# Performance work log

Measured on AMD Instinct MI355X. Metric: run time of the kernel, lower is better.

Reference implementation:

```python
import jax, jax.numpy as jnp
import numpy as np

B = 4096
D0, D1 = 256, 64


def setup_inputs() -> dict:
    key = jax.random.key(0)
    k0, k1, k2, k3 = jax.random.split(key, 4)
    return {
        "s0": jax.random.normal(k0, (B, D0), dtype=jnp.float32),
        "s1": jax.random.normal(k1, (B, D1), dtype=jnp.float32),
        "t0": jax.random.normal(k2, (B, D0), dtype=jnp.float32),
        "t1": jax.random.normal(k3, (B, D1), dtype=jnp.float32),
    }


def _gaussian_kernel(source, target):
    # feats: [2B, D]
    feats = jnp.concatenate([source, target], axis=0)
    n = feats.shape[0]
    # pairwise squared distances [2B, 2B] via the Gram-matrix identity
    # (same math as ((x - y) ** 2).sum(-1), avoids the [N, N, D] intermediate)
    sq = jnp.sum(feats * feats, axis=-1)
    dist = sq[:, None] + sq[None, :] - 2.0 * (feats @ feats.T)
    # median-heuristic bandwidth with num_kernels=1: gamma = (n^2 - n) / sum(dist)
    gamma = (n * n - n) / jnp.sum(jax.lax.stop_gradient(dist))
    return jnp.exp(-dist * gamma)


def reference(s0, s1, t0, t1):
    # joint kernel: elementwise product of per-stream Gaussian kernels
    k = _gaussian_kernel(s0, t0) * _gaussian_kernel(s1, t1)
    b = s0.shape[0]
    s2s = k[:b, :b]
    t2t = k[b:, b:]
    s2t = k[:b, b:]
    return jnp.mean(s2s + t2t - 2.0 * s2t)
```

## Files before the change

### kernel.cpp

```cpp
#include <hip/hip_runtime.h>
#include <hip/hip_fp8.h>

#define B_ROWS 4096
#define NTOT   8192
#define D0     256
#define D1     64
#define KDIM   320
#define NSB    128
#define NTILE  64
#define NTRI   2080

typedef __attribute__((ext_vector_type(4))) float f32x4;
typedef __attribute__((ext_vector_type(2))) long long2v;

#define OFF_GAM   0
#define OFF_PQ0   32
#define OFF_PQ1   544
#define OFF_P0    1056
#define OFF_P1    132128
#define OFF_R0    164896
#define OFF_R1    197664
#define OFF_BSUM  230432
#define OFF_PHI   247072

__device__ __forceinline__ void load_lds16(const void* g, void* l) {
    __builtin_amdgcn_global_load_lds(
        (const __attribute__((address_space(1))) void*)g,
        (__attribute__((address_space(3))) void*)l, 16, 0, 0);
}

__global__ __launch_bounds__(256) void k_prep(
    const float* __restrict__ s0, const float* __restrict__ s1,
    const float* __restrict__ t0, const float* __restrict__ t1,
    float* __restrict__ part0, float* __restrict__ part1,
    float* __restrict__ pq0, float* __restrict__ pq1,
    unsigned char* __restrict__ phi,
    float* __restrict__ r0vec, float* __restrict__ r1vec) {
    __shared__ float sh0[4][256];
    __shared__ float sh1[4][64];
    __shared__ float shq[4][2];
    int t = threadIdx.x, wv = t >> 6, lane = t & 63;
    int rb = blockIdx.x * 64;
    int c4 = lane * 4;
    int rr = wv;

    f32x4 cs = {0.f, 0.f, 0.f, 0.f};
    float q0 = 0.f;
    #pragma unroll 4
    for (int k = 0; k < 16; ++k) {
        int row = rb + rr + k * 4;
        const float* b0 = (row < B_ROWS) ? s0 + (size_t)row * D0 : t0 + (size_t)(row - B_ROWS) * D0;
        f32x4 v = *(const f32x4*)(b0 + c4);
        cs.x += v.x; cs.y += v.y; cs.z += v.z; cs.w += v.w;
        q0 += v.x * v.x + v.y * v.y + v.z * v.z + v.w * v.w;
    }
    *(f32x4*)&sh0[rr][c4] = cs;

    float cs1 = 0.f, q1 = 0.f;
    #pragma unroll 4
    for (int k = 0; k < 16; ++k) {
        int row = rb + rr + k * 4;
        const float* b1 = (row < B_ROWS) ? s1 + (size_t)row * D1 : t1 + (size_t)(row - B_ROWS) * D1;
        float v = b1[lane];
        cs1 += v; q1 += v * v;
    }
    sh1[rr][lane] = cs1;

    #pragma unroll
    for (int o = 32; o; o >>= 1) { q0 += __shfl_xor(q0, o, 64); q1 += __shfl_xor(q1, o, 64); }
    if (lane == 0) { shq[wv][0] = q0; shq[wv][1] = q1; }
    __syncthreads();

    part0[blockIdx.x * D0 + t] = sh0[0][t] + sh0[1][t] + sh0[2][t] + sh0[3][t];
    if (t < D1) part1[blockIdx.x * D1 + t] = sh1[0][t] + sh1[1][t] + sh1[2][t] + sh1[3][t];
    if (t == 0) {
        pq0[blockIdx.x] = shq[0][0] + shq[1][0] + shq[2][0] + shq[3][0];
        pq1[blockIdx.x] = shq[0][1] + shq[1][1] + shq[2][1] + shq[3][1];
    }

    for (int r = 0; r < 16; ++r) {
        int row = rb + wv * 16 + r;
        const float* b0p = (row < B_ROWS) ? s0 + (size_t)row * D0
                                          : t0 + (size_t)(row - B_ROWS) * D0;
        const float* b1p = (row < B_ROWS) ? s1 + (size_t)row * D1
                                          : t1 + (size_t)(row - B_ROWS) * D1;
        unsigned char* pr = phi + (size_t)row * KDIM;
        f32x4 v = *(const f32x4*)(b0p + lane * 4);
        __hip_fp8_e4m3 a0(v.x), a1(v.y), a2(v.z), a3(v.w);
        unsigned int word = (unsigned int)a0.__x | ((unsigned int)a1.__x << 8) |
                            ((unsigned int)a2.__x << 16) | ((unsigned int)a3.__x << 24);
        int doff0 = ((lane >> 4) << 6) + (((lane >> 1) & 3) << 4) +
                    (((lane >> 3) & 1) << 3) + ((lane & 1) << 2);
        *(unsigned int*)(pr + doff0) = word;
        float f0 = (float)a0, f1 = (float)a1, f2 = (float)a2, f3 = (float)a3;
        float p0 = f0 * f0 + f1 * f1 + f2 * f2 + f3 * f3;
        __hip_fp8_e4m3 qd(b1p[lane]);
        int doff1 = 256 + (((lane >> 3) & 3) << 4) + (((lane >> 5) & 1) << 3) + (lane & 7);
        pr[doff1] = qd.__x;
        float fd = (float)qd;
        float p1 = fd * fd;
        #pragma unroll
        for (int o = 32; o; o >>= 1) { p0 += __shfl_xor(p0, o, 64); p1 += __shfl_xor(p1, o, 64); }
        if (lane == 0) { r0vec[row] = p0; r1vec[row] = p1; }
    }
}

__global__ __launch_bounds__(256) void k_gamma(
    const float* __restrict__ pq0, const float* __restrict__ pq1,
    const float* __restrict__ part0, const float* __restrict__ part1,
    float* __restrict__ gam) {
    __shared__ double sh[4][4];
    int t = threadIdx.x, wv = t >> 6, lane = t & 63;

    double a0 = 0.0, a1 = 0.0;
    if (t < NSB) { a0 = (double)pq0[t]; a1 = (double)pq1[t]; }

    double F0t = 0.0;
    for (int b = 0; b < NSB; ++b) F0t += (double)part0[b * D0 + t];
    double nf0 = F0t * F0t;

    double nf1 = 0.0;
    if (t < D1) {
        double F1t = 0.0;
        for (int b = 0; b < NSB; ++b) F1t += (double)part1[b * D1 + t];
        nf1 = F1t * F1t;
    }

    #pragma unroll
    for (int o = 32; o; o >>= 1) {
        a0  += __shfl_xor(a0, o, 64);
        a1  += __shfl_xor(a1, o, 64);
        nf0 += __shfl_xor(nf0, o, 64);
        nf1 += __shfl_xor(nf1, o, 64);
    }
    if (lane == 0) { sh[wv][0] = a0; sh[wv][1] = a1; sh[wv][2] = nf0; sh[wv][3] = nf1; }
    __syncthreads();
    if (t == 0) {
        double b0 = 0, b1 = 0, b2 = 0, b3 = 0;
        for (int w = 0; w < 4; ++w) { b0 += sh[w][0]; b1 += sh[w][1]; b2 += sh[w][2]; b3 += sh[w][3]; }
        double n = (double)NTOT;
        double g0 = (n * n - n) / (2.0 * n * b0 - 2.0 * b2);
        double g1 = (n * n - n) / (2.0 * n * b1 - 2.0 * b3);
        gam[0] = (float)g0; gam[1] = (float)g1;
        gam[2] = (float)(g1 / g0); gam[3] = (float)(2.0 * g0);
    }
}

__global__ __launch_bounds__(256, 3) void k_mmd(
    const unsigned char* __restrict__ phi,
    const float* __restrict__ r0vec, const float* __restrict__ r1vec,
    const float* __restrict__ gam, double* __restrict__ blocksum) {
    int tb = (blockIdx.x & 7) * (NTRI / 8) + (blockIdx.x >> 3);
    int I = (int)((129.0f - sqrtf(16641.0f - 8.0f * (float)tb)) * 0.5f);
    while ((129 * I - I * I) / 2 > tb) --I;
    while ((129 * (I + 1) - (I + 1) * (I + 1)) / 2 <= tb) ++I;
    int J = I + (tb - (129 * I - I * I) / 2);

    __shared__ unsigned char As[24576];
    __shared__ unsigned char Bs[24576];
    __shared__ float wsum[4];

    int tid = threadIdx.x, wv = tid >> 6, lane = tid & 63;
    int wr = wv >> 1, wc = wv & 1;
    int rgrp = lane >> 4, rlow = lane & 15;
    const int rowA = I * 128, rowB = J * 128;

    const float g0 = gam[0], g1 = gam[1], ratio = gam[2], tg0 = gam[3];

    f32x4 acc_[4][4] = {};

    #define STAGE(tbase, nt)                                                    \
        _Pragma("unroll")                                                       \
        for (int it = 0; it < (nt) * 2; ++it) {                                 \
            int idx = it * 256 + tid;                                           \
            int tt = idx >> 9, rs = idx & 511;                                  \
            int row = rs >> 2, slot = rs & 3;                                   \
            int rg = slot ^ ((row >> 1) & 3);                                   \
            size_t gcol = ((tbase) + tt) * 64 + rg * 16;                        \
            load_lds16(phi + (size_t)(rowA + row) * KDIM + gcol,                \
                       As + it * 4096 + wv * 1024);                             \
            load_lds16(phi + (size_t)(rowB + row) * KDIM + gcol,                \
                       Bs + it * 4096 + wv * 1024);                             \
        }

    #define LOADFRAG(tt)                                                        \
        long2v af[4], bf[4];                                                    \
        _Pragma("unroll")                                                       \
        for (int m = 0; m < 4; ++m) {                                           \
            int row = wr * 64 + m * 16 + rlow;                                  \
            int sl = rgrp ^ ((row >> 1) & 3);                                   \
            af[m] = *(const long2v*)&As[(tt) * 8192 + row * 64 + sl * 16];      \
        }                                                                       \
        _Pragma("unroll")                                                       \
        for (int n = 0; n < 4; ++n) {                                           \
            int col = wc * 64 + n * 16 + rlow;                                  \
            int sl = rgrp ^ ((col >> 1) & 3);                                   \
            bf[n] = *(const long2v*)&Bs[(tt) * 8192 + col * 64 + sl * 16];      \
        }

    STAGE(0, 3);
    __syncthreads();
    #pragma unroll
    for (int tt = 0; tt < 3; ++tt) {
        LOADFRAG(tt);
        __builtin_amdgcn_s_setprio(1);
        #pragma unroll
        for (int m = 0; m < 4; ++m)
            #pragma unroll
            for (int n = 0; n < 4; ++n) {
                acc_[m][n] = __builtin_amdgcn_mfma_f32_16x16x32_fp8_fp8(
                    af[m][0], bf[n][0], acc_[m][n], 0, 0, 0);
                acc_[m][n] = __builtin_amdgcn_mfma_f32_16x16x32_fp8_fp8(
                    af[m][1], bf[n][1], acc_[m][n], 0, 0, 0);
            }
        __builtin_amdgcn_s_setprio(0);
    }
    __syncthreads();
    STAGE(3, 2);
    __syncthreads();
    {
        LOADFRAG(0);
        __builtin_amdgcn_s_setprio(1);
        #pragma unroll
        for (int m = 0; m < 4; ++m)
            #pragma unroll
            for (int n = 0; n < 4; ++n) {
                acc_[m][n] = __builtin_amdgcn_mfma_f32_16x16x32_fp8_fp8(
                    af[m][0], bf[n][0], acc_[m][n], 0, 0, 0);
                acc_[m][n] = __builtin_amdgcn_mfma_f32_16x16x32_fp8_fp8(
                    af[m][1], bf[n][1], acc_[m][n], 0, 0, 0);
            }
        __builtin_amdgcn_s_setprio(0);
    }
    {
        LOADFRAG(1);
        __builtin_amdgcn_s_setprio(1);
        #pragma unroll
        for (int m = 0; m < 4; ++m)
            #pragma unroll
            for (int n = 0; n < 4; ++n) {
                f32x4 tm = {0.f, 0.f, 0.f, 0.f};
                tm = __builtin_amdgcn_mfma_f32_16x16x32_fp8_fp8(
                    af[m][0], bf[n][0], tm, 0, 0, 0);
                tm = __builtin_amdgcn_mfma_f32_16x16x32_fp8_fp8(
                    af[m][1], bf[n][1], tm, 0, 0, 0);
                acc_[m][n] += ratio * tm;
            }
        __builtin_amdgcn_s_setprio(0);
    }

    float psum = 0.f;
    #pragma unroll
    for (int m = 0; m < 4; ++m) {
        int gi = rowA + wr * 64 + m * 16 + rgrp * 4;
        f32x4 r0i = *(const f32x4*)&r0vec[gi];
        f32x4 r1i = *(const f32x4*)&r1vec[gi];
        f32x4 ui = g0 * r0i + g1 * r1i;
        #pragma unroll
        for (int n = 0; n < 4; ++n) {
            int gj = rowB + wc * 64 + n * 16 + rlow;
            float uj = g0 * r0vec[gj] + g1 * r1vec[gj];
            f32x4 a = acc_[m][n];
            psum += __expf(tg0 * a.x - ui.x - uj);
            psum += __expf(tg0 * a.y - ui.y - uj);
            psum += __expf(tg0 * a.z - ui.z - uj);
            psum += __expf(tg0 * a.w - ui.w - uj);
        }
    }
    #pragma unroll
    for (int o = 32; o; o >>= 1) psum += __shfl_xor(psum, o, 64);
    if (lane == 0) wsum[wv] = psum;
    __syncthreads();
    if (tid == 0) {
        float bs = wsum[0] + wsum[1] + wsum[2] + wsum[3];
        double sgn = ((I < 32) == (J < 32)) ? 1.0 : -1.0;
        double fac = (I == J) ? 1.0 : 2.0;
        blocksum[tb] = sgn * fac * (double)bs;
    }
}

__global__ __launch_bounds__(256) void k_final(
    const double* __restrict__ blocksum, float* __restrict__ out) {
    __shared__ double sh[4];
    int t = threadIdx.x, wv = t >> 6, lane = t & 63;
    double s = 0.0;
    for (int i = t; i < NTRI; i += 256) s += blocksum[i];
    #pragma unroll
    for (int o = 32; o; o >>= 1) s += __shfl_xor(s, o, 64);
    if (lane == 0) sh[wv] = s;
    __syncthreads();
    if (t == 0) {
        double tot = sh[0] + sh[1] + sh[2] + sh[3];
        out[0] = (float)(tot / ((double)B_ROWS * (double)B_ROWS));
    }
}

extern "C" void kernel_launch(void* const* d_in, const int* in_sizes, int n_in,
                              void* d_out, int out_size, void* d_ws, size_t ws_size,
                              hipStream_t stream) {
    const float* s0 = (const float*)d_in[0];
    const float* s1 = (const float*)d_in[1];
    const float* t0 = (const float*)d_in[2];
    const float* t1 = (const float*)d_in[3];
    char* ws = (char*)d_ws;
    float*  gam  = (float*)(ws + OFF_GAM);
    float*  pq0  = (float*)(ws + OFF_PQ0);
    float*  pq1  = (float*)(ws + OFF_PQ1);
    float*  p0   = (float*)(ws + OFF_P0);
    float*  p1   = (float*)(ws + OFF_P1);
    float*  r0v  = (float*)(ws + OFF_R0);
    float*  r1v  = (float*)(ws + OFF_R1);
    double* bsum = (double*)(ws + OFF_BSUM);
    unsigned char* phi = (unsigned char*)(ws + OFF_PHI);

    k_prep<<<NSB, 256, 0, stream>>>(s0, s1, t0, t1, p0, p1, pq0, pq1, phi, r0v, r1v);
    k_gamma<<<1, 256, 0, stream>>>(pq0, pq1, p0, p1, gam);
    k_mmd<<<NTRI, 256, 0, stream>>>(phi, r0v, r1v, gam, bsum);
    k_final<<<1, 256, 0, stream>>>(bsum, (float*)d_out);
}
```

Measured before the change: 57.43 us.

## Fuse prep passes into one read, double prep blocks, stage row norms in LDS

The prep kernel now reads each input row once, computing column sums, squared norms and the fp8 quantization in the same loop. The old version made two passes over the inputs. The launch grows from 128 to 256 blocks of 32 rows each to spread the prep work, so k_gamma now reduces over 256 partials. In k_mmd the per-row bias terms g0*r0+g1*r1 are computed once into shared memory for the tile, so the epilogue reads them from LDS instead of gathering them from global memory per fragment. This adds LDS usage, and the prep change could slightly affect the occupancy of k_mmd.

After: 55.15 us. 4.0% less time.

```diff
diff --git a/kernel.cpp b/kernel.cpp
--- a/kernel.cpp
+++ b/kernel.cpp
@@ -6,7 +6,7 @@
 #define D0     256
 #define D1     64
 #define KDIM   320
-#define NSB    128
+#define PB     256
 #define NTILE  64
 #define NTRI   2080
 
@@ -14,14 +14,14 @@
 typedef __attribute__((ext_vector_type(2))) long long2v;
 
 #define OFF_GAM   0
-#define OFF_PQ0   32
-#define OFF_PQ1   544
-#define OFF_P0    1056
-#define OFF_P1    132128
-#define OFF_R0    164896
-#define OFF_R1    197664
-#define OFF_BSUM  230432
-#define OFF_PHI   247072
+#define OFF_PQ0   16
+#define OFF_PQ1   1040
+#define OFF_P0    2064
+#define OFF_P1    264208
+#define OFF_R0    329744
+#define OFF_R1    362512
+#define OFF_BSUM  395280
+#define OFF_PHI   411920
 
 __device__ __forceinline__ void load_lds16(const void* g, void* l) {
     __builtin_amdgcn_global_load_lds(
@@ -40,68 +40,56 @@
     __shared__ float sh1[4][64];
     __shared__ float shq[4][2];
     int t = threadIdx.x, wv = t >> 6, lane = t & 63;
-    int rb = blockIdx.x * 64;
-    int c4 = lane * 4;
-    int rr = wv;
-
-    f32x4 cs = {0.f, 0.f, 0.f, 0.f};
-    float q0 = 0.f;
-    #pragma unroll 4
-    for (int k = 0; k < 16; ++k) {
-        int row = rb + rr + k * 4;
-        const float* b0 = (row < B_ROWS) ? s0 + (size_t)row * D0 : t0 + (size_t)(row - B_ROWS) * D0;
-        f32x4 v = *(const f32x4*)(b0 + c4);
-        cs.x += v.x; cs.y += v.y; cs.z += v.z; cs.w += v.w;
+    int rb = blockIdx.x * 32;
+
+    int doff0 = ((lane >> 4) << 6) + (((lane >> 1) & 3) << 4) +
+                (((lane >> 3) & 1) << 3) + ((lane & 1) << 2);
+    int doff1 = 256 + (((lane >> 3) & 3) << 4) + (((lane >> 5) & 1) << 3) + (lane & 7);
+
+    f32x4 cs0 = {0.f, 0.f, 0.f, 0.f};
+    float q0 = 0.f, cs1 = 0.f, q1 = 0.f;
+
+    for (int r = 0; r < 8; ++r) {
+        int row = rb + wv * 8 + r;
+        const float* b0p = (row < B_ROWS) ? s0 + (size_t)row * D0
+                                          : t0 + (size_t)(row - B_ROWS) * D0;
+        const float* b1p = (row < B_ROWS) ? s1 + (size_t)row * D1
+                                          : t1 + (size_t)(row - B_ROWS) * D1;
+        unsigned char* pr = phi + (size_t)row * KDIM;
+
+        f32x4 v = *(const f32x4*)(b0p + lane * 4);
+        cs0.x += v.x; cs0.y += v.y; cs0.z += v.z; cs0.w += v.w;
         q0 += v.x * v.x + v.y * v.y + v.z * v.z + v.w * v.w;
-    }
-    *(f32x4*)&sh0[rr][c4] = cs;
-
-    float cs1 = 0.f, q1 = 0.f;
-    #pragma unroll 4
-    for (int k = 0; k < 16; ++k) {
-        int row = rb + rr + k * 4;
-        const float* b1 = (row < B_ROWS) ? s1 + (size_t)row * D1 : t1 + (size_t)(row - B_ROWS) * D1;
-        float v = b1[lane];
-        cs1 += v; q1 += v * v;
-    }
-    sh1[rr][lane] = cs1;
-
+        __hip_fp8_e4m3 a0(v.x), a1(v.y), a2(v.z), a3(v.w);
+        unsigned int word = (unsigned int)a0.__x | ((unsigned int)a1.__x << 8) |
+                            ((unsigned int)a2.__x << 16) | ((unsigned int)a3.__x << 24);
+        *(unsigned int*)(pr + doff0) = word;
+        float f0 = (float)a0, f1 = (float)a1, f2 = (float)a2, f3 = (float)a3;
+        float p0 = f0 * f0 + f1 * f1 + f2 * f2 + f3 * f3;
+
+        float w1 = b1p[lane];
+        cs1 += w1; q1 += w1 * w1;
+        __hip_fp8_e4m3 qd(w1);
+        pr[doff1] = qd.__x;
+        float fd = (float)qd;
+        float p1 = fd * fd;
+
+        #pragma unroll
+        for (int o = 32; o; o >>= 1) { p0 += __shfl_xor(p0, o, 64); p1 += __shfl_xor(p1, o, 64); }
+        if (lane == 0) { r0vec[row] = p0; r1vec[row] = p1; }
+    }
+
+    *(f32x4*)&sh0[wv][lane * 4] = cs0;
+    sh1[wv][lane] = cs1;
     #pragma unroll
     for (int o = 32; o; o >>= 1) { q0 += __shfl_xor(q0, o, 64); q1 += __shfl_xor(q1, o, 64); }
     if (lane == 0) { shq[wv][0] = q0; shq[wv][1] = q1; }
     __syncthreads();
-
     part0[blockIdx.x * D0 + t] = sh0[0][t] + sh0[1][t] + sh0[2][t] + sh0[3][t];
     if (t < D1) part1[blockIdx.x * D1 + t] = sh1[0][t] + sh1[1][t] + sh1[2][t] + sh1[3][t];
     if (t == 0) {
         pq0[blockIdx.x] = shq[0][0] + shq[1][0] + shq[2][0] + shq[3][0];
         pq1[blockIdx.x] = shq[0][1] + shq[1][1] + shq[2][1] + shq[3][1];
-    }
-
-    for (int r = 0; r < 16; ++r) {
-        int row = rb + wv * 16 + r;
-        const float* b0p = (row < B_ROWS) ? s0 + (size_t)row * D0
-                                          : t0 + (size_t)(row - B_ROWS) * D0;
-        const float* b1p = (row < B_ROWS) ? s1 + (size_t)row * D1
-                                          : t1 + (size_t)(row - B_ROWS) * D1;
-        unsigned char* pr = phi + (size_t)row * KDIM;
-        f32x4 v = *(const f32x4*)(b0p + lane * 4);
-        __hip_fp8_e4m3 a0(v.x), a1(v.y), a2(v.z), a3(v.w);
-        unsigned int word = (unsigned int)a0.__x | ((unsigned int)a1.__x << 8) |
-                            ((unsigned int)a2.__x << 16) | ((unsigned int)a3.__x << 24);
-        int doff0 = ((lane >> 4) << 6) + (((lane >> 1) & 3) << 4) +
-                    (((lane >> 3) & 1) << 3) + ((lane & 1) << 2);
-        *(unsigned int*)(pr + doff0) = word;
-        float f0 = (float)a0, f1 = (float)a1, f2 = (float)a2, f3 = (float)a3;
-        float p0 = f0 * f0 + f1 * f1 + f2 * f2 + f3 * f3;
-        __hip_fp8_e4m3 qd(b1p[lane]);
-        int doff1 = 256 + (((lane >> 3) & 3) << 4) + (((lane >> 5) & 1) << 3) + (lane & 7);
-        pr[doff1] = qd.__x;
-        float fd = (float)qd;
-        float p1 = fd * fd;
-        #pragma unroll
-        for (int o = 32; o; o >>= 1) { p0 += __shfl_xor(p0, o, 64); p1 += __shfl_xor(p1, o, 64); }
-        if (lane == 0) { r0vec[row] = p0; r1vec[row] = p1; }
     }
 }
 
@@ -112,17 +100,16 @@
     __shared__ double sh[4][4];
     int t = threadIdx.x, wv = t >> 6, lane = t & 63;
 
-    double a0 = 0.0, a1 = 0.0;
-    if (t < NSB) { a0 = (double)pq0[t]; a1 = (double)pq1[t]; }
+    double a0 = (double)pq0[t], a1 = (double)pq1[t];
 
     double F0t = 0.0;
-    for (int b = 0; b < NSB; ++b) F0t += (double)part0[b * D0 + t];
+    for (int b = 0; b < PB; ++b) F0t += (double)part0[b * D0 + t];
     double nf0 = F0t * F0t;
 
     double nf1 = 0.0;
     if (t < D1) {
         double F1t = 0.0;
-        for (int b = 0; b < NSB; ++b) F1t += (double)part1[b * D1 + t];
+        for (int b = 0; b < PB; ++b) F1t += (double)part1[b * D1 + t];
         nf1 = F1t * F1t;
     }
 
@@ -158,6 +145,7 @@
 
     __shared__ unsigned char As[24576];
     __shared__ unsigned char Bs[24576];
+    __shared__ float uIl[128], uJl[128];
     __shared__ float wsum[4];
 
     int tid = threadIdx.x, wv = tid >> 6, lane = tid & 63;
@@ -166,6 +154,10 @@
     const int rowA = I * 128, rowB = J * 128;
 
     const float g0 = gam[0], g1 = gam[1], ratio = gam[2], tg0 = gam[3];
+
+    if (tid < 128) uIl[tid] = g0 * r0vec[rowA + tid] + g1 * r1vec[rowA + tid];
+    else           uJl[tid - 128] = g0 * r0vec[rowB + (tid - 128)] +
+                                    g1 * r1vec[rowB + (tid - 128)];
 
     f32x4 acc_[4][4] = {};
 
@@ -252,19 +244,17 @@
     float psum = 0.f;
     #pragma unroll
     for (int m = 0; m < 4; ++m) {
-        int gi = rowA + wr * 64 + m * 16 + rgrp * 4;
-        f32x4 r0i = *(const f32x4*)&r0vec[gi];
-        f32x4 r1i = *(const f32x4*)&r1vec[gi];
-        f32x4 ui = g0 * r0i + g1 * r1i;
+        float ui[4];
+        #pragma unroll
+        for (int j = 0; j < 4; ++j) ui[j] = uIl[wr * 64 + m * 16 + rgrp * 4 + j];
         #pragma unroll
         for (int n = 0; n < 4; ++n) {
-            int gj = rowB + wc * 64 + n * 16 + rlow;
-            float uj = g0 * r0vec[gj] + g1 * r1vec[gj];
+            float uj = uJl[wc * 64 + n * 16 + rlow];
             f32x4 a = acc_[m][n];
-            psum += __expf(tg0 * a.x - ui.x - uj);
-            psum += __expf(tg0 * a.y - ui.y - uj);
-            psum += __expf(tg0 * a.z - ui.z - uj);
-            psum += __expf(tg0 * a.w - ui.w - uj);
+            psum += __expf(tg0 * a.x - ui[0] - uj);
+            psum += __expf(tg0 * a.y - ui[1] - uj);
+            psum += __expf(tg0 * a.z - ui[2] - uj);
+            psum += __expf(tg0 * a.w - ui[3] - uj);
         }
     }
     #pragma unroll
@@ -313,7 +303,7 @@
     double* bsum = (double*)(ws + OFF_BSUM);
     unsigned char* phi = (unsigned char*)(ws + OFF_PHI);
 
-    k_prep<<<NSB, 256, 0, stream>>>(s0, s1, t0, t1, p0, p1, pq0, pq1, phi, r0v, r1v);
+    k_prep<<<PB, 256, 0, stream>>>(s0, s1, t0, t1, p0, p1, pq0, pq1, phi, r0v, r1v);
     k_gamma<<<1, 256, 0, stream>>>(pq0, pq1, p0, p1, gam);
     k_mmd<<<NTRI, 256, 0, stream>>>(phi, r0v, r1v, gam, bsum);
     k_final<<<1, 256, 0, stream>>>(bsum, (float*)d_out);
```
